# Performance work log

Hardware: AMD Instinct MI355X
Metric: run time of the kernel (lower is better)

## Reference

```python
import jax, jax.numpy as jnp
import numpy as np

B, L, D, H = 2, 1024, 512, 8
h = D // H            # head_dim = 64
K = H                 # num_eigh must equal num_heads (vmap pairing in conv)
EPS = 1e-5


def _spectral_filters(seq_len: int, k: int) -> np.ndarray:
    # Hankel matrix Z_{ij} = 2 / ((i+j)^3 - (i+j)), top-k eigenvectors scaled by sigma^{1/4}
    e = np.arange(1, seq_len + 1, dtype=np.float64)
    ipj = e[:, None] + e[None, :]
    Z = 2.0 / (ipj ** 3 - ipj)
    sigma, phi = np.linalg.eigh(Z)
    sigma_k = np.clip(sigma[-k:], 1e-9, None)
    return (phi[:, -k:] * sigma_k ** 0.25).astype(np.float32)  # [L, K]


def setup_inputs() -> dict:
    key = jax.random.key(0)
    ks = jax.random.split(key, 8)
    s = 0.02
    return {
        "x": jax.random.normal(ks[0], (B, L, D), jnp.float32),
        "spectral_basis": jnp.asarray(_spectral_filters(L, K)),       # [L, K]
        "wq_w": jax.random.normal(ks[1], (D, D), jnp.float32) * s,
        "wq_b": jnp.zeros((D,), jnp.float32),
        "wk_w": jax.random.normal(ks[2], (D, D), jnp.float32) * s,
        "wk_b": jnp.zeros((D,), jnp.float32),
        "wv_w": jax.random.normal(ks[3], (D, D), jnp.float32) * s,
        "wv_b": jnp.zeros((D,), jnp.float32),
        "wo_w": jax.random.normal(ks[4], (D, D), jnp.float32) * s,
        "wo_b": jnp.zeros((D,), jnp.float32),
        "wg_w": jax.random.normal(ks[5], (h * h,), jnp.float32) * s,  # Linear(h^2 -> 1)
        "wg_b": jnp.zeros((), jnp.float32),
    }


def _causal_fft_conv(u, filt_f, n):
    # u: [B,H,L,h]; filt_f: precomputed rfft of per-head filters [H, F]
    Uf = jnp.fft.rfft(u, n=n, axis=2)                        # [B,H,F,h]
    y = jnp.fft.irfft(Uf * filt_f[None, :, :, None], n=n, axis=2)
    return y[:, :, :L]                                       # truncate full conv -> causal


def reference(x, spectral_basis, wq_w, wq_b, wk_w, wk_b, wv_w, wv_b,
              wo_w, wo_b, wg_w, wg_b):
    # projections -> [B,H,L,h]
    q = (x @ wq_w + wq_b).reshape(B, L, H, h).transpose(0, 2, 1, 3)
    k = (x @ wk_w + wk_b).reshape(B, L, H, h).transpose(0, 2, 1, 3) * h ** (-0.5)
    v = (x @ wv_w + wv_b).reshape(B, L, H, h).transpose(0, 2, 1, 3)

    n = 2 * L
    filt_f = jnp.fft.rfft(spectral_basis.T, n=n, axis=1)     # [H, F] (one filter per head)
    k_conv = _causal_fft_conv(k, filt_f, n)
    v_conv = _causal_fft_conv(v, filt_f, n)

    # gated outer product Z: [B,H,L,h,h]
    Z = jnp.einsum('bhlm,bhln->bhlmn', v_conv, k_conv)
    gate_logits = Z.reshape(B, H, L, h * h) @ wg_w + wg_b    # [B,H,L]
    gates = jax.nn.relu(gate_logits) ** 2 + EPS
    gated_Z = gates[..., None, None] * Z

    # associative scan (additive) over sequence dim
    cumul_gated_Z = jnp.cumsum(gated_Z, axis=2)              # [B,H,L,h,h]
    cumul_gates = jnp.cumsum(gates, axis=2)                  # [B,H,L]
    attn = cumul_gated_Z / (cumul_gates[..., None, None] + EPS)

    # note: original einsum sums over l (and d) independently of s
    ctxt = jnp.einsum('bhsd,bhlde->bhse', q, attn)           # [B,H,L,h]
    norm = jnp.linalg.norm(ctxt, axis=3, keepdims=True)
    unit = ctxt / jnp.maximum(norm, EPS)                     # F.normalize semantics
    out = unit.transpose(0, 2, 1, 3).reshape(B, L, D)
    return out @ wo_w + wo_b
```

## Files before the change

kernel.cpp:

```cpp
#include <hip/hip_runtime.h>
#include <math.h>


typedef __attribute__((ext_vector_type(8))) short short8;
typedef __attribute__((ext_vector_type(4))) float floatx4;

__device__ __forceinline__ unsigned short f2bf(float f) {
    unsigned int u = __float_as_uint(f);
    unsigned int r = (u + 0x7FFFu + ((u >> 16) & 1u)) >> 16;
    return (unsigned short)r;
}

__global__ __launch_bounds__(256) void k_prep(
    const float* __restrict__ x,
    const float* __restrict__ wq, const float* __restrict__ wk,
    const float* __restrict__ wv, const float* __restrict__ wo,
    const float* __restrict__ sb,
    unsigned short* __restrict__ xb,
    unsigned short* __restrict__ wT, unsigned short* __restrict__ woT,
    unsigned short* __restrict__ TB)
{
    __shared__ float sf[64][65];
    const int blk = blockIdx.x;
    const int tid = threadIdx.x;

    if (blk < 512) {
        const int gid = blk * 256 + tid;
        const float4* x4 = (const float4*)x;
        float4 a = x4[gid*2], b = x4[gid*2+1];
        uint4 o;
        o.x = f2bf(a.x) | ((unsigned)f2bf(a.y) << 16);
        o.y = f2bf(a.z) | ((unsigned)f2bf(a.w) << 16);
        o.z = f2bf(b.x) | ((unsigned)f2bf(b.y) << 16);
        o.w = f2bf(b.z) | ((unsigned)f2bf(b.w) << 16);
        ((uint4*)xb)[gid] = o;
    } else if (blk < 768) {
        const int t = blk - 512;
        const float* src; unsigned short* dst; int n0, c0, k0;
        if (t < 192) {
            int nt = t >> 3, kt = t & 7;
            n0 = nt * 64; k0 = kt * 64;
            int z = n0 >> 9; c0 = n0 & 511;
            src = (z == 0) ? wq : (z == 1) ? wk : wv;
            dst = wT;
        } else {
            int u = t - 192; int nt = u >> 3, kt = u & 7;
            n0 = nt * 64; c0 = n0; k0 = kt * 64;
            src = wo; dst = woT;
        }
        const int rr = tid >> 4, c4 = tid & 15;
        #pragma unroll
        for (int g = 0; g < 4; ++g) {
            int r = g*16 + rr;
            float4 v = *(const float4*)&src[(size_t)(k0 + r)*512 + c0 + c4*4];
            sf[r][c4*4+0]=v.x; sf[r][c4*4+1]=v.y; sf[r][c4*4+2]=v.z; sf[r][c4*4+3]=v.w;
        }
        __syncthreads();
        #pragma unroll
        for (int g = 0; g < 4; ++g) {
            int c = g*16 + rr;
            int kk = c4*4;
            ushort4 o;
            o.x = f2bf(sf[kk+0][c]); o.y = f2bf(sf[kk+1][c]);
            o.z = f2bf(sf[kk+2][c]); o.w = f2bf(sf[kk+3][c]);
            *(ushort4*)&dst[(size_t)(n0 + c)*512 + k0 + kk] = o;
        }
    } else {
        const int u = blk - 768;
        const int h = u >> 5;
        const int r0 = (u & 31) * 32;
        unsigned short* sbc = (unsigned short*)sf;
        for (int i = tid; i < 1024; i += 256)
            sbc[i] = f2bf(sb[i*8 + h]);
        __syncthreads();
        const int rr = tid >> 3, c0 = (tid & 7) * 128;
        const int t = r0 + rr;
        unsigned short* row = TB + ((size_t)h * 1024 + t) * 1024;
        for (int c = c0; c < c0 + 128; c += 8) {
            unsigned short v[8];
            #pragma unroll
            for (int j = 0; j < 8; ++j) {
                int s = c + j;
                v[j] = (t >= s) ? sbc[t - s] : (unsigned short)0;
            }
            uint4 o;
            o.x = v[0] | ((unsigned)v[1]<<16);
            o.y = v[2] | ((unsigned)v[3]<<16);
            o.z = v[4] | ((unsigned)v[5]<<16);
            o.w = v[6] | ((unsigned)v[7]<<16);
            *(uint4*)&row[c] = o;
        }
    }
}

__global__ __launch_bounds__(256) void k_qkv_mfma(
    const unsigned short* __restrict__ xb, const unsigned short* __restrict__ wT,
    const float* __restrict__ bq, const float* __restrict__ bk,
    const float* __restrict__ bv,
    float* __restrict__ qo, unsigned short* __restrict__ ub2)
{
    const int tid = threadIdx.x;
    const int lane = tid & 63, wave = tid >> 6;
    const int q = lane >> 4, ln = lane & 15;
    const int wm = wave * 32;
    const int m0 = blockIdx.y * 128;
    const int n0 = blockIdx.x * 64;

    __shared__ unsigned short As[128*40];
    __shared__ unsigned short Bs[64*40];

    floatx4 acc[2][4];
    #pragma unroll
    for (int i = 0; i < 2; ++i)
        #pragma unroll
        for (int j = 0; j < 4; ++j)
            acc[i][j] = (floatx4){0.f, 0.f, 0.f, 0.f};

    const uint4* Ag = (const uint4*)xb;
    const uint4* Bg = (const uint4*)wT;
    for (int k0 = 0; k0 < 512; k0 += 32) {
        #pragma unroll
        for (int s = 0; s < 2; ++s) {
            int c = s*256 + tid;
            int r = c >> 2, cp = c & 3;
            uint4 va = Ag[(size_t)(m0 + r)*64 + (k0 >> 3) + cp];
            *(uint4*)&As[r*40 + cp*8] = va;
        }
        {
            int r = tid >> 2, cp = tid & 3;
            uint4 vb = Bg[(size_t)(n0 + r)*64 + (k0 >> 3) + cp];
            *(uint4*)&Bs[r*40 + cp*8] = vb;
        }
        __syncthreads();
        short8 af[2], bfr[4];
        #pragma unroll
        for (int i = 0; i < 2; ++i)
            af[i]  = *(const short8*)&As[(wm + i*16 + ln)*40 + q*8];
        #pragma unroll
        for (int i = 0; i < 4; ++i)
            bfr[i] = *(const short8*)&Bs[(i*16 + ln)*40 + q*8];
        #pragma unroll
        for (int mi = 0; mi < 2; ++mi)
            #pragma unroll
            for (int ni = 0; ni < 4; ++ni)
                acc[mi][ni] = __builtin_amdgcn_mfma_f32_16x16x32_bf16(
                    af[mi], bfr[ni], acc[mi][ni], 0, 0, 0);
        __syncthreads();
    }

    const int z = n0 >> 9;
    if (z == 0) {
        #pragma unroll
        for (int mi = 0; mi < 2; ++mi) {
            #pragma unroll
            for (int ni = 0; ni < 4; ++ni) {
                int c = (n0 + ni*16 + ln) & 511;
                int head = c >> 6, dd = c & 63;
                float bb = bq[c];
                #pragma unroll
                for (int reg = 0; reg < 4; ++reg) {
                    int row = m0 + wm + mi*16 + q*4 + reg;
                    int b = row >> 10, l = row & 1023;
                    qo[(size_t)((b*8 + head)*1024 + l)*64 + dd] =
                        acc[mi][ni][reg] + bb;
                }
            }
        }
    } else {
        const float scale = (z == 1) ? 0.125f : 1.0f;
        const float* bias = (z == 1) ? bk : bv;
        unsigned short* dst = ub2 + (size_t)(z-1) * 16 * 64 * 1024;
        #pragma unroll
        for (int mi = 0; mi < 2; ++mi) {
            #pragma unroll
            for (int ni = 0; ni < 4; ++ni) {
                int c = (n0 + ni*16 + ln) & 511;
                int head = c >> 6, dd = c & 63;
                float bb = bias[c];
                int row0 = m0 + wm + mi*16 + q*4;
                int b = row0 >> 10, l0 = row0 & 1023;
                ushort4 o;
                o.x = f2bf((acc[mi][ni][0] + bb) * scale);
                o.y = f2bf((acc[mi][ni][1] + bb) * scale);
                o.z = f2bf((acc[mi][ni][2] + bb) * scale);
                o.w = f2bf((acc[mi][ni][3] + bb) * scale);
                *(ushort4*)&dst[((size_t)((b*8 + head)*64) + dd)*1024 + l0] = o;
            }
        }
    }
}

__global__ __launch_bounds__(256) void k_conv_mfma(
    const unsigned short* __restrict__ TB,
    const unsigned short* __restrict__ ub2,
    float* __restrict__ kc, float* __restrict__ vc)
{
    const int tid = threadIdx.x;
    const int lane = tid & 63, wave = tid >> 6;
    const int q = lane >> 4, ln = lane & 15;
    const int bht = blockIdx.x;
    const int it  = blockIdx.y;
    const int t0  = it * 64;
    const int bh  = bht & 15, h = bh & 7, tensor = bht >> 4;

    __shared__ unsigned short As[64*40];
    __shared__ unsigned short Bs[64*40];

    const uint4* Ag = (const uint4*)TB;
    const uint4* Bg = (const uint4*)ub2;
    const size_t abase = (size_t)h * 131072 + (size_t)t0 * 128;
    const size_t bbase = (size_t)bht * 8192;

    floatx4 acc[4];
    #pragma unroll
    for (int i = 0; i < 4; ++i) acc[i] = (floatx4){0.f,0.f,0.f,0.f};

    const int kend = t0 + 64;
    const int r = tid >> 2, cp = tid & 3;
    for (int k0 = 0; k0 < kend; k0 += 32) {
        uint4 va = Ag[abase + (size_t)r*128 + (k0 >> 3) + cp];
        uint4 vb = Bg[bbase + (size_t)r*128 + (k0 >> 3) + cp];
        *(uint4*)&As[r*40 + cp*8] = va;
        *(uint4*)&Bs[r*40 + cp*8] = vb;
        __syncthreads();
        short8 a = *(const short8*)&As[(wave*16 + ln)*40 + q*8];
        short8 b0 = *(const short8*)&Bs[(0*16 + ln)*40 + q*8];
        short8 b1 = *(const short8*)&Bs[(1*16 + ln)*40 + q*8];
        short8 b2 = *(const short8*)&Bs[(2*16 + ln)*40 + q*8];
        short8 b3 = *(const short8*)&Bs[(3*16 + ln)*40 + q*8];
        acc[0] = __builtin_amdgcn_mfma_f32_16x16x32_bf16(a, b0, acc[0], 0, 0, 0);
        acc[1] = __builtin_amdgcn_mfma_f32_16x16x32_bf16(a, b1, acc[1], 0, 0, 0);
        acc[2] = __builtin_amdgcn_mfma_f32_16x16x32_bf16(a, b2, acc[2], 0, 0, 0);
        acc[3] = __builtin_amdgcn_mfma_f32_16x16x32_bf16(a, b3, acc[3], 0, 0, 0);
        __syncthreads();
    }

    float* dst = (tensor ? vc : kc) + (size_t)bh * 65536;
    #pragma unroll
    for (int ni = 0; ni < 4; ++ni)
        #pragma unroll
        for (int reg = 0; reg < 4; ++reg) {
            int row = t0 + wave*16 + q*4 + reg;
            dst[(size_t)row*64 + ni*16 + ln] = acc[ni][reg];
        }
}

__global__ __launch_bounds__(256) void k_gate(
    const float* __restrict__ kc, const float* __restrict__ vc,
    const float* __restrict__ wg_w, const float* __restrict__ wg_b,
    float* __restrict__ gl)
{
    const int tid = threadIdx.x, tx = tid & 15, ty = tid >> 4;
    const int l0 = blockIdx.x * 64;
    const int bh = blockIdx.y;
    const float* kb = kc + (size_t)bh * 65536;
    const float* vb = vc + (size_t)bh * 65536;

    __shared__ float ks[64][17];
    __shared__ __align__(16) float wsh[16][68];
    float acc[4][4] = {};
    const float4* k4 = (const float4*)kb;
    for (int n0 = 0; n0 < 64; n0 += 16) {
        {
            int r = tid >> 2, c4 = tid & 3;
            float4 t = k4[(size_t)(l0 + r) * 16 + (n0 >> 2) + c4];
            ks[r][c4*4+0]=t.x; ks[r][c4*4+1]=t.y; ks[r][c4*4+2]=t.z; ks[r][c4*4+3]=t.w;
        }
        for (int i = tid; i < 1024; i += 256) {
            int r = i >> 6, c = i & 63;
            wsh[r][c] = wg_w[c*64 + n0 + r];
        }
        __syncthreads();
        #pragma unroll
        for (int kk = 0; kk < 16; ++kk) {
            float a[4];
            a[0] = ks[ty*4+0][kk]; a[1] = ks[ty*4+1][kk];
            a[2] = ks[ty*4+2][kk]; a[3] = ks[ty*4+3][kk];
            float4 b4 = *(const float4*)&wsh[kk][tx*4];
            float bb[4] = {b4.x, b4.y, b4.z, b4.w};
            #pragma unroll
            for (int ii = 0; ii < 4; ++ii)
                #pragma unroll
                for (int jj = 0; jj < 4; ++jj)
                    acc[ii][jj] += a[ii] * bb[jj];
        }
        __syncthreads();
    }
    __shared__ float red[64][17];
    const float wgb = wg_b[0];
    const float4* v4p = (const float4*)vb;
    #pragma unroll
    for (int i = 0; i < 4; ++i) {
        int lr = ty*4 + i;
        float4 vv = v4p[(size_t)(l0 + lr) * 16 + tx];
        red[lr][tx] = acc[i][0]*vv.x + acc[i][1]*vv.y + acc[i][2]*vv.z + acc[i][3]*vv.w;
    }
    __syncthreads();
    if (tid < 64) {
        float s = 0.0f;
        #pragma unroll
        for (int t = 0; t < 16; ++t) s += red[tid][t];
        float logit = s + wgb;
        float r = fmaxf(logit, 0.0f);
        gl[bh*1024 + l0 + tid] = r*r + 1e-5f;
    }
}

__global__ __launch_bounds__(256) void k_amat(
    const float* __restrict__ kc, const float* __restrict__ vc,
    const float* __restrict__ gl, float* __restrict__ apart)
{
    const int tid = threadIdx.x, tx = tid & 15, ty = tid >> 4;
    const int bh = blockIdx.x, slc = blockIdx.y;
    const float* kb = kc + (size_t)bh * 65536;
    const float* vb = vc + (size_t)bh * 65536;

    __shared__ float sbuf[256];
    __shared__ float wfull[1024];
    __shared__ __align__(16) float vs[16][68];
    __shared__ __align__(16) float ks2[16][68];

    {
        const float4 g4 = ((const float4*)(gl + bh*1024))[tid];
        float g[4] = {g4.x, g4.y, g4.z, g4.w};
        float p[4];
        p[0]=g[0]; p[1]=p[0]+g[1]; p[2]=p[1]+g[2]; p[3]=p[2]+g[3];
        const float s = p[3];
        sbuf[tid] = s;
        __syncthreads();
        for (int off = 1; off < 256; off <<= 1) {
            float t = (tid >= off) ? sbuf[tid-off] : 0.0f;
            __syncthreads();
            sbuf[tid] += t;
            __syncthreads();
        }
        const float base = sbuf[tid] - s;
        float r[4], pr[4];
        #pragma unroll
        for (int u = 0; u < 4; ++u) r[u] = 1.0f / (base + p[u] + 1e-5f);
        pr[0]=r[0]; pr[1]=pr[0]+r[1]; pr[2]=pr[1]+r[2]; pr[3]=pr[2]+r[3];
        const float sr = pr[3];
        __syncthreads();
        sbuf[tid] = sr;
        __syncthreads();
        for (int off = 1; off < 256; off <<= 1) {
            float t = (tid >= off) ? sbuf[tid-off] : 0.0f;
            __syncthreads();
            sbuf[tid] += t;
            __syncthreads();
        }
        const float Rtot  = sbuf[255];
        const float baser = sbuf[tid] - sr;
        wfull[tid*4+0] = g[0] * (Rtot - (baser + pr[0]) + r[0]);
        wfull[tid*4+1] = g[1] * (Rtot - (baser + pr[1]) + r[1]);
        wfull[tid*4+2] = g[2] * (Rtot - (baser + pr[2]) + r[2]);
        wfull[tid*4+3] = g[3] * (Rtot - (baser + pr[3]) + r[3]);
    }
    __syncthreads();

    float acc[4][4] = {};
    const float4* k4 = (const float4*)kb;
    const float4* v4 = (const float4*)vb;
    for (int j0 = slc*256; j0 < slc*256 + 256; j0 += 16) {
        {
            int r = tid >> 4, c4 = tid & 15;
            *(float4*)&vs[r][c4*4]  = v4[(size_t)(j0 + r)*16 + c4];
            *(float4*)&ks2[r][c4*4] = k4[(size_t)(j0 + r)*16 + c4];
        }
        __syncthreads();
        #pragma unroll
        for (int jj = 0; jj < 16; ++jj) {
            float wj = wfull[j0 + jj];
            float a[4];
            a[0] = vs[jj][ty*4+0]*wj; a[1] = vs[jj][ty*4+1]*wj;
            a[2] = vs[jj][ty*4+2]*wj; a[3] = vs[jj][ty*4+3]*wj;
            float4 b4 = *(const float4*)&ks2[jj][tx*4];
            float bb[4] = {b4.x, b4.y, b4.z, b4.w};
            #pragma unroll
            for (int ii = 0; ii < 4; ++ii)
                #pragma unroll
                for (int jc = 0; jc < 4; ++jc)
                    acc[ii][jc] += a[ii] * bb[jc];
        }
        __syncthreads();
    }
    float* ap = apart + (size_t)(slc*16 + bh) * 4096;
    #pragma unroll
    for (int i = 0; i < 4; ++i) {
        float4 o = { acc[i][0], acc[i][1], acc[i][2], acc[i][3] };
        *(float4*)&ap[(ty*4+i)*64 + tx*4] = o;
    }
}

__global__ __launch_bounds__(256) void k_ctxt(
    const float* __restrict__ q, const float* __restrict__ apart,
    unsigned short* __restrict__ ub)
{
    const int tid = threadIdx.x, tx = tid & 15, ty = tid >> 4;
    const int l0 = blockIdx.x * 64;
    const int bh = blockIdx.y;
    const float* qb = q + (size_t)bh * 65536;

    __shared__ float qs[64][17];
    __shared__ __align__(16) float As[16][68];
    float acc[4][4] = {};
    const float4* q4 = (const float4*)qb;
    const float4* a4 = (const float4*)apart;
    for (int d0 = 0; d0 < 64; d0 += 16) {
        {
            int r = tid >> 2, c4 = tid & 3;
            float4 t = q4[(size_t)(l0 + r)*16 + (d0 >> 2) + c4];
            qs[r][c4*4+0]=t.x; qs[r][c4*4+1]=t.y; qs[r][c4*4+2]=t.z; qs[r][c4*4+3]=t.w;
        }
        {
            int r = tid >> 4, c4 = tid & 15;
            size_t o = (size_t)(d0 + r)*16 + c4;
            float4 t0 = a4[(size_t)(0*16 + bh)*1024 + o];
            float4 t1 = a4[(size_t)(1*16 + bh)*1024 + o];
            float4 t2 = a4[(size_t)(2*16 + bh)*1024 + o];
            float4 t3 = a4[(size_t)(3*16 + bh)*1024 + o];
            float4 t;
            t.x = t0.x+t1.x+t2.x+t3.x; t.y = t0.y+t1.y+t2.y+t3.y;
            t.z = t0.z+t1.z+t2.z+t3.z; t.w = t0.w+t1.w+t2.w+t3.w;
            *(float4*)&As[r][c4*4] = t;
        }
        __syncthreads();
        #pragma unroll
        for (int dd = 0; dd < 16; ++dd) {
            float a[4];
            a[0] = qs[ty*4+0][dd]; a[1] = qs[ty*4+1][dd];
            a[2] = qs[ty*4+2][dd]; a[3] = qs[ty*4+3][dd];
            float4 b4 = *(const float4*)&As[dd][tx*4];
            float bb[4] = {b4.x, b4.y, b4.z, b4.w};
            #pragma unroll
            for (int ii = 0; ii < 4; ++ii)
                #pragma unroll
                for (int jj = 0; jj < 4; ++jj)
                    acc[ii][jj] += a[ii] * bb[jj];
        }
        __syncthreads();
    }
    __shared__ float red[64][17];
    __shared__ float nrm[64];
    #pragma unroll
    for (int i = 0; i < 4; ++i) {
        red[ty*4+i][tx] = acc[i][0]*acc[i][0] + acc[i][1]*acc[i][1]
                        + acc[i][2]*acc[i][2] + acc[i][3]*acc[i][3];
    }
    __syncthreads();
    if (tid < 64) {
        float s = 0.0f;
        #pragma unroll
        for (int t = 0; t < 16; ++t) s += red[tid][t];
        nrm[tid] = fmaxf(sqrtf(s), 1e-5f);
    }
    __syncthreads();
    const int b = bh >> 3, hd = bh & 7;
    #pragma unroll
    for (int i = 0; i < 4; ++i) {
        int lr = ty*4 + i;
        float inv = 1.0f / nrm[lr];
        ushort4 o;
        o.x = f2bf(acc[i][0]*inv); o.y = f2bf(acc[i][1]*inv);
        o.z = f2bf(acc[i][2]*inv); o.w = f2bf(acc[i][3]*inv);
        *(ushort4*)&ub[(size_t)(b*1024 + l0 + lr)*512 + hd*64 + tx*4] = o;
    }
}

__global__ __launch_bounds__(256) void k_out_mfma(
    const unsigned short* __restrict__ ub, const unsigned short* __restrict__ woT,
    const float* __restrict__ bo, float* __restrict__ out)
{
    const int tid = threadIdx.x;
    const int lane = tid & 63, wave = tid >> 6;
    const int q = lane >> 4, ln = lane & 15;
    const int wm = wave * 32;
    const int m0 = blockIdx.y * 128;
    const int n0 = blockIdx.x * 64;

    __shared__ unsigned short As[128*40];
    __shared__ unsigned short Bs[64*40];

    floatx4 acc[2][4];
    #pragma unroll
    for (int i = 0; i < 2; ++i)
        #pragma unroll
        for (int j = 0; j < 4; ++j)
            acc[i][j] = (floatx4){0.f, 0.f, 0.f, 0.f};

    const uint4* Ag = (const uint4*)ub;
    const uint4* Bg = (const uint4*)woT;
    for (int k0 = 0; k0 < 512; k0 += 32) {
        #pragma unroll
        for (int s = 0; s < 2; ++s) {
            int c = s*256 + tid;
            int r = c >> 2, cp = c & 3;
            uint4 va = Ag[(size_t)(m0 + r)*64 + (k0 >> 3) + cp];
            *(uint4*)&As[r*40 + cp*8] = va;
        }
        {
            int r = tid >> 2, cp = tid & 3;
            uint4 vb = Bg[(size_t)(n0 + r)*64 + (k0 >> 3) + cp];
            *(uint4*)&Bs[r*40 + cp*8] = vb;
        }
        __syncthreads();
        short8 af[2], bfr[4];
        #pragma unroll
        for (int i = 0; i < 2; ++i)
            af[i]  = *(const short8*)&As[(wm + i*16 + ln)*40 + q*8];
        #pragma unroll
        for (int i = 0; i < 4; ++i)
            bfr[i] = *(const short8*)&Bs[(i*16 + ln)*40 + q*8];
        #pragma unroll
        for (int mi = 0; mi < 2; ++mi)
            #pragma unroll
            for (int ni = 0; ni < 4; ++ni)
                acc[mi][ni] = __builtin_amdgcn_mfma_f32_16x16x32_bf16(
                    af[mi], bfr[ni], acc[mi][ni], 0, 0, 0);
        __syncthreads();
    }

    #pragma unroll
    for (int mi = 0; mi < 2; ++mi) {
        #pragma unroll
        for (int ni = 0; ni < 4; ++ni) {
            int gcol = n0 + ni*16 + ln;
            float bb = bo[gcol];
            #pragma unroll
            for (int reg = 0; reg < 4; ++reg) {
                int row = m0 + wm + mi*16 + q*4 + reg;
                out[(size_t)row*512 + gcol] = acc[mi][ni][reg] + bb;
            }
        }
    }
}

extern "C" void kernel_launch(void* const* d_in, const int* in_sizes, int n_in,
                              void* d_out, int out_size, void* d_ws, size_t ws_size,
                              hipStream_t stream)
{
    const float* x   = (const float*)d_in[0];
    const float* sb  = (const float*)d_in[1];
    const float* wq  = (const float*)d_in[2];
    const float* bq  = (const float*)d_in[3];
    const float* wk  = (const float*)d_in[4];
    const float* bk  = (const float*)d_in[5];
    const float* wv  = (const float*)d_in[6];
    const float* bv  = (const float*)d_in[7];
    const float* wo  = (const float*)d_in[8];
    const float* bo  = (const float*)d_in[9];
    const float* wg  = (const float*)d_in[10];
    const float* wgb = (const float*)d_in[11];
    float* out = (float*)d_out;
    float* ws  = (float*)d_ws;

    float* Q   = ws;
    float* KC  = ws + 1048576;
    float* VC  = ws + 2*1048576;
    float* GL  = ws + 3*1048576;
    float* AP  = GL + 16384;
    float* fp  = AP + 262144;
    unsigned short* XB  = (unsigned short*)fp;
    unsigned short* WT  = XB  + 1048576;
    unsigned short* WOT = WT  + 786432;
    unsigned short* UB  = WOT + 262144;
    unsigned short* UB2 = UB  + 1048576;
    unsigned short* TB  = UB2 + 2097152;

    k_prep     <<<dim3(1024),   256, 0, stream>>>(x, wq, wk, wv, wo, sb,
                                                  XB, WT, WOT, TB);
    k_qkv_mfma <<<dim3(24, 16), 256, 0, stream>>>(XB, WT, bq, bk, bv, Q, UB2);
    k_conv_mfma<<<dim3(32, 16), 256, 0, stream>>>(TB, UB2, KC, VC);
    k_gate     <<<dim3(16, 16), 256, 0, stream>>>(KC, VC, wg, wgb, GL);
    k_amat     <<<dim3(16, 4),  256, 0, stream>>>(KC, VC, GL, AP);
    k_ctxt     <<<dim3(16, 16), 256, 0, stream>>>(Q, AP, UB);
    k_out_mfma <<<dim3(8, 16),  256, 0, stream>>>(UB, WOT, bo, out);
}
```

Before: 164.3 us.

## Move gate bilinear to bf16 MFMA and split amat reduction across more slices

The gate logit computation k^T W v is now done with bf16 MFMA: k_conv also writes a bf16 copy of the k-convolution, and k_prep gains a block that converts the gate weights to bf16. A wave shuffle reduction then forms the dot with v. Separately, k_amat's sequence reduction is split into 8 slices instead of 4, which doubles its grid and the partial-sum buffer, and k_ctxt now sums 8 partials. This trades fp32 FMA work and low parallelism for lower gate precision, extra bf16 writes and more partial-sum traffic.

```diff
diff --git a/kernel.cpp b/kernel.cpp
--- a/kernel.cpp
+++ b/kernel.cpp
@@ -15,10 +15,10 @@
     const float* __restrict__ x,
     const float* __restrict__ wq, const float* __restrict__ wk,
     const float* __restrict__ wv, const float* __restrict__ wo,
-    const float* __restrict__ sb,
+    const float* __restrict__ sb, const float* __restrict__ wg,
     unsigned short* __restrict__ xb,
     unsigned short* __restrict__ wT, unsigned short* __restrict__ woT,
-    unsigned short* __restrict__ TB)
+    unsigned short* __restrict__ TB, unsigned short* __restrict__ wgb)
 {
     __shared__ float sf[64][65];
     const int blk = blockIdx.x;
@@ -65,7 +65,7 @@
             o.z = f2bf(sf[kk+2][c]); o.w = f2bf(sf[kk+3][c]);
             *(ushort4*)&dst[(size_t)(n0 + c)*512 + k0 + kk] = o;
         }
-    } else {
+    } else if (blk < 1024) {
         const int u = blk - 768;
         const int h = u >> 5;
         const int r0 = (u & 31) * 32;
@@ -89,6 +89,17 @@
             o.z = v[4] | ((unsigned)v[5]<<16);
             o.w = v[6] | ((unsigned)v[7]<<16);
             *(uint4*)&row[c] = o;
+        }
+    } else {
+        const float4* wg4 = (const float4*)wg;
+        for (int i = tid; i < 512; i += 256) {
+            float4 a = wg4[i*2], b = wg4[i*2+1];
+            uint4 o;
+            o.x = f2bf(a.x) | ((unsigned)f2bf(a.y) << 16);
+            o.y = f2bf(a.z) | ((unsigned)f2bf(a.w) << 16);
+            o.z = f2bf(b.x) | ((unsigned)f2bf(b.y) << 16);
+            o.w = f2bf(b.z) | ((unsigned)f2bf(b.w) << 16);
+            ((uint4*)wgb)[i] = o;
         }
     }
 }
@@ -193,7 +204,8 @@
 __global__ __launch_bounds__(256) void k_conv_mfma(
     const unsigned short* __restrict__ TB,
     const unsigned short* __restrict__ ub2,
-    float* __restrict__ kc, float* __restrict__ vc)
+    float* __restrict__ kc, float* __restrict__ vc,
+    unsigned short* __restrict__ kcb)
 {
     const int tid = threadIdx.x;
     const int lane = tid & 63, wave = tid >> 6;
@@ -243,66 +255,81 @@
             int row = t0 + wave*16 + q*4 + reg;
             dst[(size_t)row*64 + ni*16 + ln] = acc[ni][reg];
         }
-}
-
-__global__ __launch_bounds__(256) void k_gate(
-    const float* __restrict__ kc, const float* __restrict__ vc,
-    const float* __restrict__ wg_w, const float* __restrict__ wg_b,
+    if (!tensor) {
+        unsigned short* db = kcb + (size_t)bh * 65536;
+        #pragma unroll
+        for (int ni = 0; ni < 4; ++ni)
+            #pragma unroll
+            for (int reg = 0; reg < 4; ++reg) {
+                int row = t0 + wave*16 + q*4 + reg;
+                db[(size_t)row*64 + ni*16 + ln] = f2bf(acc[ni][reg]);
+            }
+    }
+}
+
+__global__ __launch_bounds__(256) void k_gate_mfma(
+    const unsigned short* __restrict__ kcb, const float* __restrict__ vc,
+    const unsigned short* __restrict__ wgb, const float* __restrict__ wg_b,
     float* __restrict__ gl)
 {
-    const int tid = threadIdx.x, tx = tid & 15, ty = tid >> 4;
+    const int tid = threadIdx.x;
+    const int lane = tid & 63, wave = tid >> 6;
+    const int q = lane >> 4, ln = lane & 15;
     const int l0 = blockIdx.x * 64;
     const int bh = blockIdx.y;
-    const float* kb = kc + (size_t)bh * 65536;
+
+    __shared__ unsigned short As[64*72];
+    __shared__ unsigned short Bs[64*72];
+
+    const uint4* Ag = (const uint4*)(kcb + (size_t)bh * 65536);
+    const uint4* Bg = (const uint4*)wgb;
+    #pragma unroll
+    for (int s = 0; s < 2; ++s) {
+        int idx = s*256 + tid;
+        int r = idx >> 3, cp = idx & 7;
+        *(uint4*)&As[r*72 + cp*8] = Ag[(size_t)(l0 + r)*8 + cp];
+        *(uint4*)&Bs[r*72 + cp*8] = Bg[r*8 + cp];
+    }
+    __syncthreads();
+
+    floatx4 T[4];
+    #pragma unroll
+    for (int mt = 0; mt < 4; ++mt) T[mt] = (floatx4){0.f,0.f,0.f,0.f};
+    #pragma unroll
+    for (int k0 = 0; k0 < 64; k0 += 32) {
+        short8 a = *(const short8*)&As[(wave*16 + ln)*72 + k0 + q*8];
+        #pragma unroll
+        for (int mt = 0; mt < 4; ++mt) {
+            short8 b = *(const short8*)&Bs[(mt*16 + ln)*72 + k0 + q*8];
+            T[mt] = __builtin_amdgcn_mfma_f32_16x16x32_bf16(a, b, T[mt], 0, 0, 0);
+        }
+    }
+
     const float* vb = vc + (size_t)bh * 65536;
-
-    __shared__ float ks[64][17];
-    __shared__ __align__(16) float wsh[16][68];
-    float acc[4][4] = {};
-    const float4* k4 = (const float4*)kb;
-    for (int n0 = 0; n0 < 64; n0 += 16) {
-        {
-            int r = tid >> 2, c4 = tid & 3;
-            float4 t = k4[(size_t)(l0 + r) * 16 + (n0 >> 2) + c4];
-            ks[r][c4*4+0]=t.x; ks[r][c4*4+1]=t.y; ks[r][c4*4+2]=t.z; ks[r][c4*4+3]=t.w;
-        }
-        for (int i = tid; i < 1024; i += 256) {
-            int r = i >> 6, c = i & 63;
-            wsh[r][c] = wg_w[c*64 + n0 + r];
-        }
-        __syncthreads();
-        #pragma unroll
-        for (int kk = 0; kk < 16; ++kk) {
-            float a[4];
-            a[0] = ks[ty*4+0][kk]; a[1] = ks[ty*4+1][kk];
-            a[2] = ks[ty*4+2][kk]; a[3] = ks[ty*4+3][kk];
-            float4 b4 = *(const float4*)&wsh[kk][tx*4];
-            float bb[4] = {b4.x, b4.y, b4.z, b4.w};
-            #pragma unroll
-            for (int ii = 0; ii < 4; ++ii)
-                #pragma unroll
-                for (int jj = 0; jj < 4; ++jj)
-                    acc[ii][jj] += a[ii] * bb[jj];
-        }
-        __syncthreads();
-    }
-    __shared__ float red[64][17];
-    const float wgb = wg_b[0];
-    const float4* v4p = (const float4*)vb;
-    #pragma unroll
-    for (int i = 0; i < 4; ++i) {
-        int lr = ty*4 + i;
-        float4 vv = v4p[(size_t)(l0 + lr) * 16 + tx];
-        red[lr][tx] = acc[i][0]*vv.x + acc[i][1]*vv.y + acc[i][2]*vv.z + acc[i][3]*vv.w;
-    }
-    __syncthreads();
-    if (tid < 64) {
-        float s = 0.0f;
-        #pragma unroll
-        for (int t = 0; t < 16; ++t) s += red[tid][t];
-        float logit = s + wgb;
-        float r = fmaxf(logit, 0.0f);
-        gl[bh*1024 + l0 + tid] = r*r + 1e-5f;
+    float part[4] = {0.f, 0.f, 0.f, 0.f};
+    #pragma unroll
+    for (int mt = 0; mt < 4; ++mt)
+        #pragma unroll
+        for (int reg = 0; reg < 4; ++reg) {
+            int l = l0 + wave*16 + q*4 + reg;
+            part[reg] += T[mt][reg] * vb[(size_t)l*64 + mt*16 + ln];
+        }
+    #pragma unroll
+    for (int reg = 0; reg < 4; ++reg) {
+        part[reg] += __shfl_xor(part[reg], 1);
+        part[reg] += __shfl_xor(part[reg], 2);
+        part[reg] += __shfl_xor(part[reg], 4);
+        part[reg] += __shfl_xor(part[reg], 8);
+    }
+    if (ln == 0) {
+        const float wgbias = wg_b[0];
+        #pragma unroll
+        for (int reg = 0; reg < 4; ++reg) {
+            int l = l0 + wave*16 + q*4 + reg;
+            float s = part[reg] + wgbias;
+            float rr = fmaxf(s, 0.0f);
+            gl[bh*1024 + l] = rr*rr + 1e-5f;
+        }
     }
 }
 
@@ -361,7 +388,7 @@
     float acc[4][4] = {};
     const float4* k4 = (const float4*)kb;
     const float4* v4 = (const float4*)vb;
-    for (int j0 = slc*256; j0 < slc*256 + 256; j0 += 16) {
+    for (int j0 = slc*128; j0 < slc*128 + 128; j0 += 16) {
         {
             int r = tid >> 4, c4 = tid & 15;
             *(float4*)&vs[r][c4*4]  = v4[(size_t)(j0 + r)*16 + c4];
@@ -415,13 +442,12 @@
         {
             int r = tid >> 4, c4 = tid & 15;
             size_t o = (size_t)(d0 + r)*16 + c4;
-            float4 t0 = a4[(size_t)(0*16 + bh)*1024 + o];
-            float4 t1 = a4[(size_t)(1*16 + bh)*1024 + o];
-            float4 t2 = a4[(size_t)(2*16 + bh)*1024 + o];
-            float4 t3 = a4[(size_t)(3*16 + bh)*1024 + o];
-            float4 t;
-            t.x = t0.x+t1.x+t2.x+t3.x; t.y = t0.y+t1.y+t2.y+t3.y;
-            t.z = t0.z+t1.z+t2.z+t3.z; t.w = t0.w+t1.w+t2.w+t3.w;
+            float4 t = a4[(size_t)(0*16 + bh)*1024 + o];
+            #pragma unroll
+            for (int s = 1; s < 8; ++s) {
+                float4 u = a4[(size_t)(s*16 + bh)*1024 + o];
+                t.x += u.x; t.y += u.y; t.z += u.z; t.w += u.w;
+            }
             *(float4*)&As[r][c4*4] = t;
         }
         __syncthreads();
@@ -559,20 +585,22 @@
     float* VC  = ws + 2*1048576;
     float* GL  = ws + 3*1048576;
     float* AP  = GL + 16384;
-    float* fp  = AP + 262144;
+    float* fp  = AP + 524288;
     unsigned short* XB  = (unsigned short*)fp;
     unsigned short* WT  = XB  + 1048576;
     unsigned short* WOT = WT  + 786432;
     unsigned short* UB  = WOT + 262144;
     unsigned short* UB2 = UB  + 1048576;
     unsigned short* TB  = UB2 + 2097152;
-
-    k_prep     <<<dim3(1024),   256, 0, stream>>>(x, wq, wk, wv, wo, sb,
-                                                  XB, WT, WOT, TB);
+    unsigned short* WGB = TB  + 8388608;
+    unsigned short* KCB = WGB + 4096;
+
+    k_prep     <<<dim3(1025),   256, 0, stream>>>(x, wq, wk, wv, wo, sb, wg,
+                                                  XB, WT, WOT, TB, WGB);
     k_qkv_mfma <<<dim3(24, 16), 256, 0, stream>>>(XB, WT, bq, bk, bv, Q, UB2);
-    k_conv_mfma<<<dim3(32, 16), 256, 0, stream>>>(TB, UB2, KC, VC);
-    k_gate     <<<dim3(16, 16), 256, 0, stream>>>(KC, VC, wg, wgb, GL);
-    k_amat     <<<dim3(16, 4),  256, 0, stream>>>(KC, VC, GL, AP);
+    k_conv_mfma<<<dim3(32, 16), 256, 0, stream>>>(TB, UB2, KC, VC, KCB);
+    k_gate_mfma<<<dim3(16, 16), 256, 0, stream>>>(KCB, VC, WGB, wgb, GL);
+    k_amat     <<<dim3(16, 8),  256, 0, stream>>>(KC, VC, GL, AP);
     k_ctxt     <<<dim3(16, 16), 256, 0, stream>>>(Q, AP, UB);
     k_out_mfma <<<dim3(8, 16),  256, 0, stream>>>(UB, WOT, bo, out);
 }
```

Result: faster. 154.5 us (-6.0%).
